# Kernel tuning notes

Hardware: AMD Instinct MI355X
Metric: run time of the kernel (lower is better)

The kernel has to match this reference:

```python
import jax, jax.numpy as jnp
import numpy as np
from jax import lax

EPS = 1e-5  # BatchNorm eps (torch default)

def _up2_bilinear_ac(x):
    # bilinear upsample x2, align_corners=True; x: [B,C,H,W]
    B, C, H, W = x.shape
    def axis_interp(n_in, n_out):
        pos = jnp.arange(n_out, dtype=jnp.float32) * ((n_in - 1) / (n_out - 1))
        i0 = jnp.floor(pos).astype(jnp.int32)
        i1 = jnp.minimum(i0 + 1, n_in - 1)
        w = (pos - i0.astype(jnp.float32)).astype(x.dtype)
        return i0, i1, w
    i0, i1, wh = axis_interp(H, 2 * H)
    x = x[:, :, i0, :] * (1.0 - wh)[None, None, :, None] + x[:, :, i1, :] * wh[None, None, :, None]
    j0, j1, ww = axis_interp(W, 2 * W)
    x = x[:, :, :, j0] * (1.0 - ww) + x[:, :, :, j1] * ww
    return x

def setup_inputs() -> dict:
    key = jax.random.key(0)
    ks = jax.random.split(key, 8)
    B, Cin, Cout, H, W = 8, 64, 32, 128, 128
    att, K = 16, 2  # attention_channel = max(int(64*0.0625),16)=16; kernel_num=2
    n = lambda k, s, sc: jax.random.normal(k, s, jnp.float32) * sc
    return {
        'x': n(ks[0], (B, Cin, H, W), 1.0),
        'fc_w': n(ks[1], (att, Cin), 0.1),
        'bn_a_gamma': jnp.ones((att,), jnp.float32), 'bn_a_beta': jnp.zeros((att,), jnp.float32),
        'bn_a_mean': jnp.zeros((att,), jnp.float32), 'bn_a_var': jnp.ones((att,), jnp.float32),
        'ch_w': n(ks[2], (Cin, att), 0.1), 'ch_b': jnp.zeros((Cin,), jnp.float32),
        'fil_w': n(ks[3], (Cout, att), 0.1), 'fil_b': jnp.zeros((Cout,), jnp.float32),
        'sp_w': n(ks[4], (9, att), 0.1), 'sp_b': jnp.zeros((9,), jnp.float32),
        'k_w': n(ks[5], (K, att), 0.1), 'k_b': jnp.zeros((K,), jnp.float32),
        'weight': n(ks[6], (K, Cout, Cin, 3, 3), 0.05),
        'bn_gamma': jnp.ones((Cout,), jnp.float32), 'bn_beta': jnp.zeros((Cout,), jnp.float32),
        'bn_mean': jnp.zeros((Cout,), jnp.float32), 'bn_var': jnp.ones((Cout,), jnp.float32),
    }

def reference(x, fc_w, bn_a_gamma, bn_a_beta, bn_a_mean, bn_a_var,
              ch_w, ch_b, fil_w, fil_b, sp_w, sp_b, k_w, k_b,
              weight, bn_gamma, bn_beta, bn_mean, bn_var):
    x = _up2_bilinear_ac(x)
    B, Cin, H, W = x.shape
    K, Cout = weight.shape[0], weight.shape[1]
    # --- ODConv attention branch (on GAP features) ---
    g = x.mean(axis=(2, 3))                                    # [B,Cin]
    h = g @ fc_w.T                                             # [B,att]
    h = (h - bn_a_mean) / jnp.sqrt(bn_a_var + EPS) * bn_a_gamma + bn_a_beta
    h = jax.nn.relu(h)
    ch_att = jax.nn.sigmoid(h @ ch_w.T + ch_b)                 # [B,Cin]
    fil_att = jax.nn.sigmoid(h @ fil_w.T + fil_b)              # [B,Cout]
    sp_att = jax.nn.sigmoid(h @ sp_w.T + sp_b).reshape(B, 1, 1, 1, 3, 3)
    k_att = jax.nn.softmax(h @ k_w.T + k_b, axis=1).reshape(B, K, 1, 1, 1, 1)
    # per-sample aggregated filters: [B,Cout,Cin,3,3]
    agg_w = jnp.sum(k_att * sp_att * weight[None], axis=1)
    # --- dynamic conv (per-sample filter), channel-attended input ---
    x = x * ch_att[:, :, None, None]
    def conv1(xi, wi):
        return lax.conv_general_dilated(xi[None], wi, (1, 1), [(1, 1), (1, 1)],
                                        dimension_numbers=('NCHW', 'OIHW', 'NCHW'))[0]
    y = jax.vmap(conv1)(x, agg_w)                              # [B,Cout,H,W]
    y = y * fil_att[:, :, None, None]
    # --- BatchNorm2d (inference) + GELU (exact erf) ---
    y = (y - bn_mean[:, None, None]) / jnp.sqrt(bn_var[:, None, None] + EPS)
    y = y * bn_gamma[:, None, None] + bn_beta[:, None, None]
    return jax.nn.gelu(y, approximate=False)
```

## Files before the change

kernel.cpp:

```cpp
#include <hip/hip_runtime.h>
#include <hip/hip_bf16.h>

#define EPSBN 1e-5f

typedef short short8 __attribute__((ext_vector_type(8)));
typedef float f32x16 __attribute__((ext_vector_type(16)));

static __device__ __forceinline__ unsigned short f2u(float f){
  __hip_bfloat16 h = __float2bfloat16(f);
  union { __hip_bfloat16 h; unsigned short u; } c; c.h = h; return c.u;
}

#define WS_G     2048
#define WS_S     7168
#define WS_T     8192
#define WS_AGGB  16384

__global__ __launch_bounds__(256) void k_gap(const float* __restrict__ x, float* __restrict__ g){
  __shared__ float w[128];
  __shared__ float partial[4];
  int tid = threadIdx.x;
  if (tid < 128){
    int i = tid;
    float s = 0.f;
    int rstart = max(0, (int)floorf((float)(i-1)*(255.0f/127.0f)));
    #pragma unroll
    for (int k = 0; k < 8; ++k){
      int r = rstart + k;
      if (r <= 255){
        float pos = (float)r * (127.0f/255.0f);
        int i0 = (int)pos; float fr = pos - (float)i0; int i1 = min(i0+1,127);
        if (i0 == i) s += 1.0f - fr;
        if (i1 == i) s += fr;
      }
    }
    w[i] = s;
  }
  __syncthreads();
  const float4* xp = (const float4*)(x + ((size_t)blockIdx.x << 14));
  float s = 0.f;
  for (int gi = tid; gi < 4096; gi += 256){
    int i = gi >> 5, j4 = (gi & 31) * 4;
    float4 v = xp[gi];
    s += (v.x*w[j4] + v.y*w[j4+1] + v.z*w[j4+2] + v.w*w[j4+3]) * w[i];
  }
  for (int off = 32; off > 0; off >>= 1) s += __shfl_down(s, off, 64);
  if ((tid & 63) == 0) partial[tid >> 6] = s;
  __syncthreads();
  if (tid == 0) g[blockIdx.x] = (partial[0]+partial[1]+partial[2]+partial[3]) * (1.0f/65536.0f);
}

__global__ __launch_bounds__(256) void k_aggw(const float* __restrict__ g,
                      const float* __restrict__ fc_w,
                      const float* __restrict__ bga, const float* __restrict__ bba,
                      const float* __restrict__ bma, const float* __restrict__ bva,
                      const float* __restrict__ ch_w, const float* __restrict__ ch_b,
                      const float* __restrict__ fil_w, const float* __restrict__ fil_b,
                      const float* __restrict__ sp_w, const float* __restrict__ sp_b,
                      const float* __restrict__ k_w, const float* __restrict__ k_b,
                      const float* __restrict__ bn_g, const float* __restrict__ bn_b,
                      const float* __restrict__ bn_m, const float* __restrict__ bn_v,
                      const float* __restrict__ weight,
                      unsigned short* __restrict__ aggb,
                      float* __restrict__ sS, float* __restrict__ tT)
{
  __shared__ float h[8][16];
  int tid = threadIdx.x;
  if (tid < 128){
    int b = tid >> 4, a = tid & 15;
    float acc = 0.f;
    for (int c = 0; c < 64; ++c) acc += g[b*64+c] * fc_w[a*64+c];
    float v = (acc - bma[a]) * rsqrtf(bva[a] + EPSBN) * bga[a] + bba[a];
    h[b][a] = fmaxf(v, 0.f);
  }
  __syncthreads();

  int idx = blockIdx.x*256 + tid;
  int ci_l = idx & 15;
  int o    = (idx >> 4) & 31;
  int s    = (idx >> 9) % 9;
  int t2   = idx / 4608;
  int cc   = t2 & 3, b = t2 >> 2;
  int ci   = cc*16 + ci_l;

  const float* hb = h[b];
  float zc = ch_b[ci], zs = sp_b[s];
  float z0 = k_b[0],  z1 = k_b[1];
  #pragma unroll
  for (int a = 0; a < 16; ++a){
    float hv = hb[a];
    zc += hv*ch_w[ci*16+a];
    zs += hv*sp_w[s*16+a];
    z0 += hv*k_w[a];
    z1 += hv*k_w[16+a];
  }
  float chv = 1.f/(1.f+expf(-zc));
  float spv = 1.f/(1.f+expf(-zs));
  float m = fmaxf(z0,z1);
  float e0 = expf(z0-m), e1 = expf(z1-m), inv = 1.f/(e0+e1);
  float ka0 = e0*inv, ka1 = e1*inv;
  float w0 = weight[(o*64+ci)*9+s];
  float w1 = weight[((32+o)*64+ci)*9+s];
  aggb[idx] = f2u(chv*spv*(ka0*w0 + ka1*w1));

  if (blockIdx.x == 0){
    int bb = tid >> 5, oo = tid & 31;
    float z = fil_b[oo];
    #pragma unroll
    for (int a = 0; a < 16; ++a) z += h[bb][a]*fil_w[oo*16+a];
    float f = 1.f/(1.f+expf(-z));
    float invs = rsqrtf(bn_v[oo] + EPSBN);
    sS[tid] = f * bn_g[oo] * invs;
    if (bb == 0) tT[oo] = bn_b[oo] - bn_m[oo]*bn_g[oo]*invs;
  }
}

__global__ __launch_bounds__(256) void k_conv(const float* __restrict__ x,
                                              const unsigned short* __restrict__ aggb,
                                              const float* __restrict__ sS,
                                              const float* __restrict__ tT,
                                              float* __restrict__ out)
{
  __shared__ unsigned short xt[18*18*24];
  __shared__ unsigned short wt[288*24];
  __shared__ float xin[16*121];
  __shared__ int   ir0s[18], ir1s[18], jc0s[18], jc1s[18];
  __shared__ float rwhs[18], cwws[18];
  __shared__ float sSs[32], tTs[32];

  int tid = threadIdx.x;
  int bi  = blockIdx.x;
  int b   = bi >> 8, t = bi & 255;
  int p0  = (t >> 4) * 16, q0 = (t & 15) * 16;
  int lane = tid & 63, wv = tid >> 6;
  if (tid < 32){ sSs[tid] = sS[b*32+tid]; tTs[tid] = tT[tid]; }

  int i0b = (int)((float)max(p0-1,0) * (127.0f/255.0f));
  int j0b = (int)((float)max(q0-1,0) * (127.0f/255.0f));

  if (tid < 18){
    int gr = p0 - 1 + tid;
    if ((unsigned)gr < 256u){
      float pos = (float)gr * (127.0f/255.0f);
      int i0 = (int)pos;
      ir0s[tid] = i0 - i0b;
      ir1s[tid] = min(i0+1,127) - i0b;
      rwhs[tid] = pos - (float)i0;
    } else { ir0s[tid] = -1000; ir1s[tid] = 0; rwhs[tid] = 0.f; }
  } else if (tid < 36){
    int k = tid - 18;
    int gq = q0 - 1 + k;
    if ((unsigned)gq < 256u){
      float pos = (float)gq * (127.0f/255.0f);
      int j0 = (int)pos;
      jc0s[k] = j0 - j0b;
      jc1s[k] = min(j0+1,127) - j0b;
      cwws[k] = pos - (float)j0;
    } else { jc0s[k] = -1000; jc1s[k] = 0; cwws[k] = 0.f; }
  }

  f32x16 acc[2];
  #pragma unroll
  for (int i = 0; i < 16; ++i){ acc[0][i] = 0.f; acc[1][i] = 0.f; }

  int n  = lane & 31;
  int kq = lane >> 5;

  for (int cc = 0; cc < 4; ++cc){
    __syncthreads();
    {
      const float* xb = x + (((size_t)(b*64 + cc*16)) << 14);
      for (int e = tid; e < 1920; e += 256){
        int ci  = e / 120;
        int rem = e - ci*120;
        int ir  = rem / 12;
        int jj  = rem - ir*12;
        int row = min(i0b + ir, 127);
        int col = min(j0b + jj, 127);
        xin[ci*121 + rem] = xb[((size_t)ci << 14) + (row << 7) + col];
      }
    }
    for (int e = tid; e < 576; e += 256){
      int so = e >> 1, half = e & 1;
      size_t gidx = (((size_t)(b*4+cc)*288 + so) << 4) + half*8;
      *(short8*)&wt[so*24 + half*8] = *(const short8*)&aggb[gidx];
    }
    __syncthreads();
    for (int e = tid; e < 5184; e += 256){
      int ci   = e & 15;
      int rest = e >> 4;
      int rr   = rest / 18;
      int qq   = rest - rr*18;
      unsigned short uv = 0;
      int i0 = ir0s[rr], j0 = jc0s[qq];
      if (i0 >= 0 && j0 >= 0){
        int i1 = ir1s[rr], j1 = jc1s[qq];
        float wh = rwhs[rr], ww = cwws[qq];
        const float* base = &xin[ci*121];
        float v00 = base[i0*12+j0], v01 = base[i0*12+j1];
        float v10 = base[i1*12+j0], v11 = base[i1*12+j1];
        float a0 = v00 + (v01 - v00)*ww;
        float a1 = v10 + (v11 - v10)*ww;
        uv = f2u(a0 + (a1 - a0)*wh);
      }
      xt[(rr*18+qq)*24 + ci] = uv;
    }
    __syncthreads();

    #pragma unroll
    for (int s = 0; s < 9; ++s){
      const int ky = s / 3, kx = s % 3;
      short8 av = *(const short8*)&wt[(s*32 + n)*24 + kq*8];
      #pragma unroll
      for (int tt = 0; tt < 2; ++tt){
        int lr = 2*(2*wv + tt) + (n >> 4);
        int rr = lr + ky;
        int qq = (n & 15) + kx;
        short8 bv = *(const short8*)&xt[(rr*18+qq)*24 + kq*8];
        acc[tt] = __builtin_amdgcn_mfma_f32_32x32x16_bf16(av, bv, acc[tt], 0, 0, 0);
      }
    }
  }

  #pragma unroll
  for (int tt = 0; tt < 2; ++tt){
    int lr = 2*(2*wv + tt) + (n >> 4);
    int p = p0 + lr, q = q0 + (n & 15);
    #pragma unroll
    for (int r = 0; r < 16; ++r){
      int o = (r & 3) + 8*(r >> 2) + 4*kq;
      float val = acc[tt][r]*sSs[o] + tTs[o];
      float gl  = 0.5f*val*(1.f + erff(val*0.70710678118f));
      out[(((size_t)(b*32+o)) << 16) + (p << 8) + q] = gl;
    }
  }
}

extern "C" void kernel_launch(void* const* d_in, const int* in_sizes, int n_in,
                              void* d_out, int out_size, void* d_ws, size_t ws_size,
                              hipStream_t stream)
{
  const float* x     = (const float*)d_in[0];
  const float* fc_w  = (const float*)d_in[1];
  const float* bga   = (const float*)d_in[2];
  const float* bba   = (const float*)d_in[3];
  const float* bma   = (const float*)d_in[4];
  const float* bva   = (const float*)d_in[5];
  const float* ch_w  = (const float*)d_in[6];
  const float* ch_b  = (const float*)d_in[7];
  const float* fil_w = (const float*)d_in[8];
  const float* fil_b = (const float*)d_in[9];
  const float* sp_w  = (const float*)d_in[10];
  const float* sp_b  = (const float*)d_in[11];
  const float* k_w   = (const float*)d_in[12];
  const float* k_b   = (const float*)d_in[13];
  const float* weight= (const float*)d_in[14];
  const float* bn_g  = (const float*)d_in[15];
  const float* bn_b  = (const float*)d_in[16];
  const float* bn_m  = (const float*)d_in[17];
  const float* bn_v  = (const float*)d_in[18];

  char* ws = (char*)d_ws;
  float* g   = (float*)(ws + WS_G);
  float* sS  = (float*)(ws + WS_S);
  float* tT  = (float*)(ws + WS_T);
  unsigned short* aggb = (unsigned short*)(ws + WS_AGGB);
  float* out = (float*)d_out;

  hipLaunchKernelGGL(k_gap,  dim3(512),  dim3(256), 0, stream, x, g);
  hipLaunchKernelGGL(k_aggw, dim3(576),  dim3(256), 0, stream, g, fc_w, bga, bba, bma, bva,
                     ch_w, ch_b, fil_w, fil_b, sp_w, sp_b, k_w, k_b,
                     bn_g, bn_b, bn_m, bn_v, weight, aggb, sS, tT);
  hipLaunchKernelGGL(k_conv, dim3(2048), dim3(256), 0, stream, x, aggb, sS, tT, out);
}
```

Before: 206.9 us.

## Precompute bilinear upsample into bf16 channel-last buffer before conv

Adds a separate k_up kernel that upsamples the whole input once into a bf16 NHWC-like buffer with 32-channel groups. The conv kernel then loads ready-made bf16 tiles with vector loads instead of recomputing bilinear interpolation per tile with halo overlap. It also processes 32 input channels per stage (two MFMA k-steps) with a padded LDS stride, which halves the number of sync rounds. In exchange it adds an extra kernel launch and writes and reads roughly 67MB of extra intermediate bf16 traffic.

```diff
diff --git a/kernel.cpp b/kernel.cpp
--- a/kernel.cpp
+++ b/kernel.cpp
@@ -15,6 +15,7 @@
 #define WS_S     7168
 #define WS_T     8192
 #define WS_AGGB  16384
+#define WS_XUP   327680
 
 __global__ __launch_bounds__(256) void k_gap(const float* __restrict__ x, float* __restrict__ g){
   __shared__ float w[128];
@@ -76,12 +77,12 @@
   __syncthreads();
 
   int idx = blockIdx.x*256 + tid;
-  int ci_l = idx & 15;
-  int o    = (idx >> 4) & 31;
-  int s    = (idx >> 9) % 9;
-  int t2   = idx / 4608;
-  int cc   = t2 & 3, b = t2 >> 2;
-  int ci   = cc*16 + ci_l;
+  int ci_l = idx & 31;
+  int o    = (idx >> 5) & 31;
+  int s    = (idx >> 10) % 9;
+  int t2   = (idx >> 10) / 9;
+  int cc   = t2 & 1, b = t2 >> 1;
+  int ci   = cc*32 + ci_l;
 
   const float* hb = h[b];
   float zc = ch_b[ci], zs = sp_b[s];
@@ -115,17 +116,71 @@
   }
 }
 
-__global__ __launch_bounds__(256) void k_conv(const float* __restrict__ x,
+__global__ __launch_bounds__(256) void k_up(const float* __restrict__ x,
+                                            unsigned int* __restrict__ xup32)
+{
+  __shared__ float xin[16*798];
+  int tid = threadIdx.x;
+  int bi  = blockIdx.x;
+  int strip = bi & 31, h16 = (bi >> 5) & 3, b = bi >> 7;
+  int r0 = strip * 8;
+  int i0b = (int)((float)r0 * (127.0f/255.0f));
+
+  for (int e = tid; e < 12288; e += 256){
+    int ir = e >> 11, rem = e & 2047, ci = rem >> 7, j = rem & 127;
+    int row = min(i0b + ir, 127);
+    xin[ci*798 + ir*133 + j] = x[(((size_t)(b*64 + h16*16 + ci)) << 14) + (row << 7) + j];
+  }
+  __syncthreads();
+
+  int ci2 = tid & 7, cbase = tid >> 3;
+  int j0t[8], j1t[8]; float wwt[8];
+  #pragma unroll
+  for (int jj = 0; jj < 8; ++jj){
+    int c = cbase + 32*jj;
+    float pos = (float)c * (127.0f/255.0f);
+    int j0 = (int)pos;
+    j0t[jj] = j0; j1t[jj] = min(j0+1,127); wwt[jj] = pos - (float)j0;
+  }
+  const float* base0 = &xin[(ci2*2+0)*798];
+  const float* base1 = &xin[(ci2*2+1)*798];
+  size_t pxbase = ((size_t)(b*2 + (h16>>1))) << 16;
+  int halfoff = (h16 & 1)*8;
+
+  for (int rr = 0; rr < 8; ++rr){
+    int r = r0 + rr;
+    float posr = (float)r * (127.0f/255.0f);
+    int i0 = (int)posr; float wh = posr - (float)i0;
+    int ir0 = (i0 - i0b)*133, ir1 = (min(i0+1,127) - i0b)*133;
+    #pragma unroll
+    for (int jj = 0; jj < 8; ++jj){
+      int c = cbase + 32*jj;
+      int j0 = j0t[jj], j1 = j1t[jj]; float ww = wwt[jj];
+      float v00 = base0[ir0+j0], v01 = base0[ir0+j1];
+      float v10 = base0[ir1+j0], v11 = base0[ir1+j1];
+      float a0 = v00 + (v01-v00)*ww;
+      float a1 = v10 + (v11-v10)*ww;
+      float r0v = a0 + (a1-a0)*wh;
+      float u00 = base1[ir0+j0], u01 = base1[ir0+j1];
+      float u10 = base1[ir1+j0], u11 = base1[ir1+j1];
+      float b0 = u00 + (u01-u00)*ww;
+      float b1 = u10 + (u11-u10)*ww;
+      float r1v = b0 + (b1-b0)*wh;
+      unsigned pack = (unsigned)f2u(r0v) | (((unsigned)f2u(r1v)) << 16);
+      xup32[(pxbase + (size_t)(r*256 + c))*16 + halfoff + ci2] = pack;
+    }
+  }
+}
+
+#define XT_STRIDE 40
+__global__ __launch_bounds__(256) void k_conv(const unsigned short* __restrict__ xup,
                                               const unsigned short* __restrict__ aggb,
                                               const float* __restrict__ sS,
                                               const float* __restrict__ tT,
                                               float* __restrict__ out)
 {
-  __shared__ unsigned short xt[18*18*24];
-  __shared__ unsigned short wt[288*24];
-  __shared__ float xin[16*121];
-  __shared__ int   ir0s[18], ir1s[18], jc0s[18], jc1s[18];
-  __shared__ float rwhs[18], cwws[18];
+  __shared__ unsigned short xt[18*18*XT_STRIDE];
+  __shared__ unsigned short wt[288*XT_STRIDE];
   __shared__ float sSs[32], tTs[32];
 
   int tid = threadIdx.x;
@@ -135,28 +190,15 @@
   int lane = tid & 63, wv = tid >> 6;
   if (tid < 32){ sSs[tid] = sS[b*32+tid]; tTs[tid] = tT[tid]; }
 
-  int i0b = (int)((float)max(p0-1,0) * (127.0f/255.0f));
-  int j0b = (int)((float)max(q0-1,0) * (127.0f/255.0f));
-
-  if (tid < 18){
-    int gr = p0 - 1 + tid;
-    if ((unsigned)gr < 256u){
-      float pos = (float)gr * (127.0f/255.0f);
-      int i0 = (int)pos;
-      ir0s[tid] = i0 - i0b;
-      ir1s[tid] = min(i0+1,127) - i0b;
-      rwhs[tid] = pos - (float)i0;
-    } else { ir0s[tid] = -1000; ir1s[tid] = 0; rwhs[tid] = 0.f; }
-  } else if (tid < 36){
-    int k = tid - 18;
-    int gq = q0 - 1 + k;
-    if ((unsigned)gq < 256u){
-      float pos = (float)gq * (127.0f/255.0f);
-      int j0 = (int)pos;
-      jc0s[k] = j0 - j0b;
-      jc1s[k] = min(j0+1,127) - j0b;
-      cwws[k] = pos - (float)j0;
-    } else { jc0s[k] = -1000; jc1s[k] = 0; cwws[k] = 0.f; }
+  int ldsoff[6], gmoff[6]; bool val[6];
+  int cnt = (tid < 16) ? 6 : 5;
+  for (int k = 0; k < cnt; ++k){
+    int e = tid + (k << 8);
+    int rr = e / 72; int rem = e - rr*72; int qq = rem >> 2; int gq4 = rem & 3;
+    int gr = p0 - 1 + rr, gq = q0 - 1 + qq;
+    val[k]    = ((unsigned)gr < 256u) && ((unsigned)gq < 256u);
+    ldsoff[k] = (rr*18+qq)*XT_STRIDE + gq4*8;
+    gmoff[k]  = (gr*256+gq)*32 + gq4*8;
   }
 
   f32x16 acc[2];
@@ -166,58 +208,34 @@
   int n  = lane & 31;
   int kq = lane >> 5;
 
-  for (int cc = 0; cc < 4; ++cc){
-    __syncthreads();
-    {
-      const float* xb = x + (((size_t)(b*64 + cc*16)) << 14);
-      for (int e = tid; e < 1920; e += 256){
-        int ci  = e / 120;
-        int rem = e - ci*120;
-        int ir  = rem / 12;
-        int jj  = rem - ir*12;
-        int row = min(i0b + ir, 127);
-        int col = min(j0b + jj, 127);
-        xin[ci*121 + rem] = xb[((size_t)ci << 14) + (row << 7) + col];
-      }
-    }
-    for (int e = tid; e < 576; e += 256){
-      int so = e >> 1, half = e & 1;
-      size_t gidx = (((size_t)(b*4+cc)*288 + so) << 4) + half*8;
-      *(short8*)&wt[so*24 + half*8] = *(const short8*)&aggb[gidx];
-    }
-    __syncthreads();
-    for (int e = tid; e < 5184; e += 256){
-      int ci   = e & 15;
-      int rest = e >> 4;
-      int rr   = rest / 18;
-      int qq   = rest - rr*18;
-      unsigned short uv = 0;
-      int i0 = ir0s[rr], j0 = jc0s[qq];
-      if (i0 >= 0 && j0 >= 0){
-        int i1 = ir1s[rr], j1 = jc1s[qq];
-        float wh = rwhs[rr], ww = cwws[qq];
-        const float* base = &xin[ci*121];
-        float v00 = base[i0*12+j0], v01 = base[i0*12+j1];
-        float v10 = base[i1*12+j0], v11 = base[i1*12+j1];
-        float a0 = v00 + (v01 - v00)*ww;
-        float a1 = v10 + (v11 - v10)*ww;
-        uv = f2u(a0 + (a1 - a0)*wh);
-      }
-      xt[(rr*18+qq)*24 + ci] = uv;
+  for (int cc = 0; cc < 2; ++cc){
+    if (cc) __syncthreads();
+    const unsigned short* xb = xup + (((size_t)(b*2+cc)) << 21);
+    for (int k = 0; k < cnt; ++k){
+      short8 v = {0,0,0,0,0,0,0,0};
+      if (val[k]) v = *(const short8*)&xb[gmoff[k]];
+      *(short8*)&xt[ldsoff[k]] = v;
+    }
+    const unsigned short* wbg = aggb + ((size_t)(b*2+cc))*9216;
+    for (int e = tid; e < 1152; e += 256){
+      *(short8*)&wt[(e >> 2)*XT_STRIDE + (e & 3)*8] = *(const short8*)&wbg[e*8];
     }
     __syncthreads();
 
     #pragma unroll
     for (int s = 0; s < 9; ++s){
       const int ky = s / 3, kx = s % 3;
-      short8 av = *(const short8*)&wt[(s*32 + n)*24 + kq*8];
       #pragma unroll
-      for (int tt = 0; tt < 2; ++tt){
-        int lr = 2*(2*wv + tt) + (n >> 4);
-        int rr = lr + ky;
-        int qq = (n & 15) + kx;
-        short8 bv = *(const short8*)&xt[(rr*18+qq)*24 + kq*8];
-        acc[tt] = __builtin_amdgcn_mfma_f32_32x32x16_bf16(av, bv, acc[tt], 0, 0, 0);
+      for (int k2 = 0; k2 < 2; ++k2){
+        short8 av = *(const short8*)&wt[(s*32 + n)*XT_STRIDE + k2*16 + kq*8];
+        #pragma unroll
+        for (int tt = 0; tt < 2; ++tt){
+          int lr = 2*(2*wv + tt) + (n >> 4);
+          int rr = lr + ky;
+          int qq = (n & 15) + kx;
+          short8 bv = *(const short8*)&xt[(rr*18+qq)*XT_STRIDE + k2*16 + kq*8];
+          acc[tt] = __builtin_amdgcn_mfma_f32_32x32x16_bf16(av, bv, acc[tt], 0, 0, 0);
+        }
       }
     }
   }
@@ -229,8 +247,8 @@
     #pragma unroll
     for (int r = 0; r < 16; ++r){
       int o = (r & 3) + 8*(r >> 2) + 4*kq;
-      float val = acc[tt][r]*sSs[o] + tTs[o];
-      float gl  = 0.5f*val*(1.f + erff(val*0.70710678118f));
+      float valv = acc[tt][r]*sSs[o] + tTs[o];
+      float gl  = 0.5f*valv*(1.f + erff(valv*0.70710678118f));
       out[(((size_t)(b*32+o)) << 16) + (p << 8) + q] = gl;
     }
   }
@@ -265,11 +283,13 @@
   float* sS  = (float*)(ws + WS_S);
   float* tT  = (float*)(ws + WS_T);
   unsigned short* aggb = (unsigned short*)(ws + WS_AGGB);
+  unsigned short* xup  = (unsigned short*)(ws + WS_XUP);
   float* out = (float*)d_out;
 
   hipLaunchKernelGGL(k_gap,  dim3(512),  dim3(256), 0, stream, x, g);
   hipLaunchKernelGGL(k_aggw, dim3(576),  dim3(256), 0, stream, g, fc_w, bga, bba, bma, bva,
                      ch_w, ch_b, fil_w, fil_b, sp_w, sp_b, k_w, k_b,
                      bn_g, bn_b, bn_m, bn_v, weight, aggb, sS, tT);
-  hipLaunchKernelGGL(k_conv, dim3(2048), dim3(256), 0, stream, x, aggb, sS, tT, out);
-}
+  hipLaunchKernelGGL(k_up,   dim3(1024), dim3(256), 0, stream, x, (unsigned int*)xup);
+  hipLaunchKernelGGL(k_conv, dim3(2048), dim3(256), 0, stream, xup, aggb, sS, tT, out);
+}
```

New measurement: 206.8 us. About the same (-0.0%).
